# Performance work log

Measured on AMD Instinct MI355X. Metric: run time of the kernel, lower is better.

Reference implementation:

```python
import jax, jax.numpy as jnp
import numpy as np

# Config (matches init_kwargs)
D_MODEL = 1024
D_MLP = 4096
N_EXPERTS = 8
TOP_K = 2  # experts_per_token
BATCH = 1
POS = 2048


def setup_inputs() -> dict:
    key = jax.random.key(0)
    k0, k1, k2, k3, k4 = jax.random.split(key, 5)
    s = 0.02  # typical init scale
    x = jax.random.normal(k0, (BATCH, POS, D_MODEL), jnp.float32)
    W_gate = jax.random.normal(k1, (D_MODEL, N_EXPERTS), jnp.float32) * s  # router
    We_gate = jax.random.normal(k2, (N_EXPERTS, D_MODEL, D_MLP), jnp.float32) * s
    We_in = jax.random.normal(k3, (N_EXPERTS, D_MODEL, D_MLP), jnp.float32) * s
    We_out = jax.random.normal(k4, (N_EXPERTS, D_MLP, D_MODEL), jnp.float32) * s
    return {"x": x, "W_gate": W_gate, "We_gate": We_gate, "We_in": We_in, "We_out": We_out}


def reference(x, W_gate, We_gate, We_in, We_out):
    B, P, D = x.shape
    T = B * P
    E = W_gate.shape[1]
    h = x.reshape(T, D)  # [T, D]

    # Router: logits -> fp32 softmax -> top-k -> renormalize (as in torch code)
    logits = h @ W_gate  # [T, E]
    probs = jax.nn.softmax(logits.astype(jnp.float32), axis=-1)
    topw, topi = jax.lax.top_k(probs, TOP_K)  # [T, K]
    topw = topw / jnp.sum(topw, axis=-1, keepdims=True)
    topw = topw.astype(x.dtype)

    # Per-token combine weight for each expert (0 if not routed). [T, E]
    w_full = jnp.zeros((T, E), x.dtype).at[jnp.arange(T)[:, None], topi].add(topw)

    # Gated-MLP per expert; scan over the small fixed expert axis to avoid
    # materializing [E, T, D_MLP] hidden states at once.
    def per_expert(acc, params):
        Wg, Wi, Wo, we = params  # Wg/Wi: [D, D_MLP], Wo: [D_MLP, D], we: [T]
        hid = jax.nn.silu(h @ Wg) * (h @ Wi)  # [T, D_MLP]
        return acc + (hid @ Wo) * we[:, None], None

    res, _ = jax.lax.scan(
        per_expert,
        jnp.zeros((T, D), x.dtype),
        (We_gate, We_in, We_out, w_full.T),
    )
    return res.reshape(B, P, D)
```

## Files before the change

### kernel.cpp

```cpp
#include <hip/hip_runtime.h>
#include <hip/hip_bf16.h>

#define T_TOK 2048
#define DMODEL 1024
#define DMLP 4096
#define NEXP 8

typedef __bf16 bf16x8 __attribute__((ext_vector_type(8)));
typedef float f32x4 __attribute__((ext_vector_type(4)));

__device__ __forceinline__ unsigned short f2bf(float f) {
  return __builtin_bit_cast(unsigned short, (__bf16)f);
}

__device__ __forceinline__ void gload16(const unsigned short* g,
                                        unsigned short* l) {
  __builtin_amdgcn_global_load_lds(
      (const __attribute__((address_space(1))) unsigned int*)g,
      (__attribute__((address_space(3))) unsigned int*)l, 16, 0, 0);
}

__global__ __launch_bounds__(64) void router_k(
    const float* __restrict__ x, const float* __restrict__ wg,
    int* __restrict__ topi, float* __restrict__ topw,
    unsigned short* __restrict__ xb) {
  int t = blockIdx.x;
  int lane = threadIdx.x;
  const float* hx = x + (size_t)t * DMODEL;
  float acc[NEXP];
#pragma unroll
  for (int e = 0; e < NEXP; ++e) acc[e] = 0.f;
  for (int i = lane; i < DMODEL; i += 64) {
    float xi = hx[i];
    if (xb) xb[(size_t)t * DMODEL + i] = f2bf(xi);
    const float* w = wg + (size_t)i * NEXP;
#pragma unroll
    for (int e = 0; e < NEXP; ++e) acc[e] += xi * w[e];
  }
#pragma unroll
  for (int off = 32; off > 0; off >>= 1) {
#pragma unroll
    for (int e = 0; e < NEXP; ++e) acc[e] += __shfl_down(acc[e], off);
  }
  if (lane == 0) {
    float m = acc[0];
#pragma unroll
    for (int e = 1; e < NEXP; ++e) m = fmaxf(m, acc[e]);
    float p[NEXP], s = 0.f;
#pragma unroll
    for (int e = 0; e < NEXP; ++e) { p[e] = expf(acc[e] - m); s += p[e]; }
    float inv = 1.f / s;
#pragma unroll
    for (int e = 0; e < NEXP; ++e) p[e] *= inv;
    int i1 = 0;
#pragma unroll
    for (int e = 1; e < NEXP; ++e) if (p[e] > p[i1]) i1 = e;
    int i2 = (i1 == 0) ? 1 : 0;
#pragma unroll
    for (int e = 0; e < NEXP; ++e) if (e != i1 && p[e] > p[i2]) i2 = e;
    float w1 = p[i1], w2 = p[i2];
    float rs = 1.f / (w1 + w2);
    topi[2 * t] = i1;
    topi[2 * t + 1] = i2;
    topw[2 * t] = w1 * rs;
    topw[2 * t + 1] = w2 * rs;
  }
}

__global__ __launch_bounds__(512) void compact_k(
    const int* __restrict__ topi, const float* __restrict__ topw,
    int* __restrict__ offsets, int* __restrict__ perm,
    float* __restrict__ wrow, int* __restrict__ inv) {
  int tid = threadIdx.x;
  int e = tid >> 6, lane = tid & 63;
  __shared__ unsigned char st[2 * T_TOK];
  __shared__ int scnt[NEXP];
  __shared__ int soff[NEXP + 1];
  for (int i = tid; i < (2 * T_TOK) / 4; i += 512) {
    int4 v = ((const int4*)topi)[i];
    uchar4 u;
    u.x = (unsigned char)v.x; u.y = (unsigned char)v.y;
    u.z = (unsigned char)v.z; u.w = (unsigned char)v.w;
    ((uchar4*)st)[i] = u;
  }
  __syncthreads();
  int c = 0;
  for (int j = lane; j < 2 * T_TOK; j += 64) {
    unsigned long long m = __ballot(st[j] == e);
    c += __popcll(m);
  }
  if (lane == 0) scnt[e] = c;
  __syncthreads();
  if (tid == 0) {
    int s = 0;
    for (int k = 0; k < NEXP; ++k) { soff[k] = s; s += scnt[k]; }
    soff[NEXP] = s;
    for (int k = 0; k <= NEXP; ++k) offsets[k] = soff[k];
  }
  __syncthreads();
  int base = soff[e];
  for (int j = lane; j < 2 * T_TOK; j += 64) {
    bool f = (st[j] == e);
    unsigned long long m = __ballot(f);
    if (f) {
      int p = base + __popcll(m & ((1ULL << lane) - 1ULL));
      perm[p] = j >> 1;
      wrow[p] = topw[j];
      inv[j] = p;
    }
    base += __popcll(m);
  }
}

template <int SK, int SN>
__global__ __launch_bounds__(256) void tpose_k(
    const float* __restrict__ src0, unsigned short* __restrict__ dst0) {
  int e = blockIdx.z;
  const float* src = src0 + (size_t)e * SK * SN;
  unsigned short* dst = dst0 + (size_t)e * SK * SN;
  int k0 = blockIdx.y * 64, c0 = blockIdx.x * 64;
  __shared__ unsigned short tl[64 * 64];
  int tid = threadIdx.x;
  int j = tid & 15, g = tid >> 4;
  int c4 = j * 4, r0 = g * 4;
  const float* sp = src + (size_t)(k0 + r0) * SN + c0 + c4;
  float4 v0 = *(const float4*)(sp);
  float4 v1 = *(const float4*)(sp + SN);
  float4 v2 = *(const float4*)(sp + 2 * SN);
  float4 v3 = *(const float4*)(sp + 3 * SN);
  const float* p0 = (const float*)&v0;
  const float* p1 = (const float*)&v1;
  const float* p2 = (const float*)&v2;
  const float* p3 = (const float*)&v3;
#pragma unroll
  for (int i = 0; i < 4; ++i) {
    int c = c4 + i;
    ushort4 u;
    u.x = f2bf(p0[i]); u.y = f2bf(p1[i]);
    u.z = f2bf(p2[i]); u.w = f2bf(p3[i]);
    int sw = ((c >> 2) & 14) << 2;
    *(ushort4*)(&tl[c * 64 + (r0 ^ sw)]) = u;
  }
  __syncthreads();
#pragma unroll
  for (int i = 0; i < 2; ++i) {
    int task = tid + i * 256;
    int rr = task >> 3, cc = task & 7;
    int sw = ((rr >> 2) & 14) << 2;
    uint4 w = *(const uint4*)(&tl[rr * 64 + ((cc * 8) ^ sw)]);
    *(uint4*)(dst + (size_t)(c0 + rr) * SK + k0 + cc * 8) = w;
  }
}

__global__ __launch_bounds__(256) void hid2_k(
    const unsigned short* __restrict__ xb, const unsigned short* __restrict__ wgt,
    const unsigned short* __restrict__ wit, const int* __restrict__ offsets,
    const int* __restrict__ perm, const float* __restrict__ wrow,
    unsigned short* __restrict__ hid) {
  int e = blockIdx.z;
  int off = offsets[e], end = offsets[e + 1];
  int cnt = end - off;
  int m0 = blockIdx.y * 128;
  if (m0 >= cnt) return;
  int nb = blockIdx.x * 64;

  __shared__ unsigned short As[128 * 32];
  __shared__ unsigned short Bs[128 * 32];

  int tid = threadIdx.x;
  int lane = tid & 63, wid = tid >> 6;
  int wm = (wid & 1) * 64, wn = (wid >> 1) * 64;
  int lr = lane & 15, q = lane >> 4;

  f32x4 acc[4][4];
  f32x4 z = {0.f, 0.f, 0.f, 0.f};
#pragma unroll
  for (int i = 0; i < 4; ++i)
#pragma unroll
    for (int j = 0; j < 4; ++j) acc[i][j] = z;

  const unsigned short* aptr[2];
  const unsigned short* bptr[2];
#pragma unroll
  for (int it = 0; it < 2; ++it) {
    int task = tid + it * 256;
    int r = task >> 2, ch = task & 3;
    int pl = m0 + r;
    int src = perm[off + ((pl < cnt) ? pl : 0)];
    aptr[it] = xb + (size_t)src * DMODEL + ch * 8;
    int arr = (r >> 5) & 1;
    int col = nb + (r & 31) + ((r >> 6) << 5);
    const unsigned short* w =
        (arr ? wit : wgt) + (size_t)e * DMLP * DMODEL;
    bptr[it] = w + (size_t)col * DMODEL + ch * 8;
  }

  for (int k0 = 0; k0 < DMODEL; k0 += 32) {
#pragma unroll
    for (int it = 0; it < 2; ++it) {
      gload16(aptr[it] + k0, &As[(tid + it * 256) * 8]);
      gload16(bptr[it] + k0, &Bs[(tid + it * 256) * 8]);
    }
    __syncthreads();
    bf16x8 af[4], bfr[4];
#pragma unroll
    for (int i = 0; i < 4; ++i)
      af[i] = *(const bf16x8*)(&As[(wm + i * 16 + lr) * 32 + q * 8]);
#pragma unroll
    for (int j = 0; j < 4; ++j)
      bfr[j] = *(const bf16x8*)(&Bs[(wn + j * 16 + lr) * 32 + q * 8]);
#pragma unroll
    for (int i = 0; i < 4; ++i)
#pragma unroll
      for (int j = 0; j < 4; ++j)
        acc[i][j] = __builtin_amdgcn_mfma_f32_16x16x32_bf16(af[i], bfr[j],
                                                            acc[i][j], 0, 0, 0);
    __syncthreads();
  }

  int colbase = nb + (wn ? 32 : 0);
#pragma unroll
  for (int i = 0; i < 4; ++i) {
#pragma unroll
    for (int jp = 0; jp < 2; ++jp) {
#pragma unroll
      for (int r = 0; r < 4; ++r) {
        int row = wm + i * 16 + q * 4 + r;
        int pl = m0 + row;
        if (pl < cnt) {
          int pos = off + pl;
          float g = acc[i][jp][r], vv = acc[i][jp + 2][r];
          float hv = (g / (1.f + expf(-g))) * vv * wrow[pos];
          hid[(size_t)pos * DMLP + colbase + jp * 16 + lr] = f2bf(hv);
        }
      }
    }
  }
}

__global__ __launch_bounds__(256) void out2_k(
    const unsigned short* __restrict__ hid, const unsigned short* __restrict__ wot,
    const int* __restrict__ offsets, float* __restrict__ tmp) {
  int e = blockIdx.z;
  int off = offsets[e], end = offsets[e + 1];
  int cnt = end - off;
  int m0 = blockIdx.y * 128;
  if (m0 >= cnt) return;
  int n0 = blockIdx.x * 128;

  __shared__ unsigned short As[128 * 32];
  __shared__ unsigned short Bs[128 * 32];

  int tid = threadIdx.x;
  int lane = tid & 63, wid = tid >> 6;
  int wm = (wid & 1) * 64, wn = (wid >> 1) * 64;
  int lr = lane & 15, q = lane >> 4;

  f32x4 acc[4][4];
  f32x4 z = {0.f, 0.f, 0.f, 0.f};
#pragma unroll
  for (int i = 0; i < 4; ++i)
#pragma unroll
    for (int j = 0; j < 4; ++j) acc[i][j] = z;

  const unsigned short* aptr[2];
  const unsigned short* bptr[2];
#pragma unroll
  for (int it = 0; it < 2; ++it) {
    int task = tid + it * 256;
    int r = task >> 2, ch = task & 3;
    int pl = m0 + r;
    aptr[it] = hid + (size_t)(off + ((pl < cnt) ? pl : 0)) * DMLP + ch * 8;
    bptr[it] = wot + (size_t)e * DMODEL * DMLP + (size_t)(n0 + r) * DMLP + ch * 8;
  }

  for (int k0 = 0; k0 < DMLP; k0 += 32) {
#pragma unroll
    for (int it = 0; it < 2; ++it) {
      gload16(aptr[it] + k0, &As[(tid + it * 256) * 8]);
      gload16(bptr[it] + k0, &Bs[(tid + it * 256) * 8]);
    }
    __syncthreads();
    bf16x8 af[4], bfr[4];
#pragma unroll
    for (int i = 0; i < 4; ++i)
      af[i] = *(const bf16x8*)(&As[(wm + i * 16 + lr) * 32 + q * 8]);
#pragma unroll
    for (int j = 0; j < 4; ++j)
      bfr[j] = *(const bf16x8*)(&Bs[(wn + j * 16 + lr) * 32 + q * 8]);
#pragma unroll
    for (int i = 0; i < 4; ++i)
#pragma unroll
      for (int j = 0; j < 4; ++j)
        acc[i][j] = __builtin_amdgcn_mfma_f32_16x16x32_bf16(af[i], bfr[j],
                                                            acc[i][j], 0, 0, 0);
    __syncthreads();
  }

#pragma unroll
  for (int i = 0; i < 4; ++i)
#pragma unroll
    for (int j = 0; j < 4; ++j)
#pragma unroll
      for (int r = 0; r < 4; ++r) {
        int row = wm + i * 16 + q * 4 + r;
        int pl = m0 + row;
        if (pl < cnt) {
          tmp[(size_t)(off + pl) * DMODEL + n0 + wn + j * 16 + lr] =
              acc[i][j][r];
        }
      }
}

__global__ __launch_bounds__(256) void comb_k(const float* __restrict__ tmp,
                                              const int* __restrict__ inv,
                                              float* __restrict__ out) {
  int t = blockIdx.x, c = threadIdx.x;
  int i0 = inv[2 * t], i1 = inv[2 * t + 1];
  const float4* t4 = (const float4*)tmp;
  float4 a = t4[(size_t)i0 * 256 + c];
  float4 b = t4[(size_t)i1 * 256 + c];
  float4 o;
  o.x = a.x + b.x; o.y = a.y + b.y; o.z = a.z + b.z; o.w = a.w + b.w;
  ((float4*)out)[(size_t)t * 256 + c] = o;
}

#define BPITCH 40

__global__ __launch_bounds__(256) void hid_k(
    const float* __restrict__ x, const float* __restrict__ weg,
    const float* __restrict__ wei, const int* __restrict__ offsets,
    const int* __restrict__ perm, const float* __restrict__ wrow,
    unsigned short* __restrict__ hid) {
  int e = blockIdx.z;
  int off = offsets[e], end = offsets[e + 1];
  int cnt = end - off;
  int m0 = blockIdx.y * 128;
  if (m0 >= cnt) return;
  int nb = blockIdx.x * 64;
  const float* wg = weg + (size_t)e * DMODEL * DMLP;
  const float* wi = wei + (size_t)e * DMODEL * DMLP;

  __shared__ unsigned short As[128 * BPITCH];
  __shared__ unsigned short Bg[64 * BPITCH];
  __shared__ unsigned short Bi[64 * BPITCH];

  int tid = threadIdx.x;
  int lane = tid & 63, wid = tid >> 6;
  int wm = (wid & 1) * 64, wn = (wid >> 1) * 32;
  int lr = lane & 15, q = lane >> 4;

  f32x4 accg[4][2], acci[4][2];
  f32x4 z = {0.f, 0.f, 0.f, 0.f};
#pragma unroll
  for (int i = 0; i < 4; ++i)
#pragma unroll
    for (int j = 0; j < 2; ++j) { accg[i][j] = z; acci[i][j] = z; }

  const float* aptr[4];
  int adst[4];
#pragma unroll
  for (int it = 0; it < 4; ++it) {
    int task = tid + it * 256;
    int r = task >> 3, kc = (task & 7) * 4;
    int pl = m0 + r;
    int src = perm[off + ((pl < cnt) ? pl : 0)];
    aptr[it] = x + (size_t)src * DMODEL + kc;
    adst[it] = r * BPITCH + kc;
  }
  int tn = (tid & 15) * 4, tk = (tid >> 4) * 2;

  for (int k0 = 0; k0 < DMODEL; k0 += 32) {
#pragma unroll
    for (int it = 0; it < 4; ++it) {
      float4 v = *(const float4*)(aptr[it] + k0);
      ushort4 u;
      u.x = f2bf(v.x); u.y = f2bf(v.y); u.z = f2bf(v.z); u.w = f2bf(v.w);
      *(ushort4*)(&As[adst[it]]) = u;
    }
    {
      const float* pg = wg + (size_t)(k0 + tk) * DMLP + nb + tn;
      float4 g0 = *(const float4*)(pg);
      float4 g1 = *(const float4*)(pg + DMLP);
      const float* pi = wi + (size_t)(k0 + tk) * DMLP + nb + tn;
      float4 i0 = *(const float4*)(pi);
      float4 i1 = *(const float4*)(pi + DMLP);
      const float* c0 = (const float*)&g0;
      const float* c1 = (const float*)&g1;
      const float* d0 = (const float*)&i0;
      const float* d1 = (const float*)&i1;
#pragma unroll
      for (int cix = 0; cix < 4; ++cix) {
        ushort2 vg; vg.x = f2bf(c0[cix]); vg.y = f2bf(c1[cix]);
        *(ushort2*)(&Bg[(tn + cix) * BPITCH + tk]) = vg;
        ushort2 vi; vi.x = f2bf(d0[cix]); vi.y = f2bf(d1[cix]);
        *(ushort2*)(&Bi[(tn + cix) * BPITCH + tk]) = vi;
      }
    }
    __syncthreads();
    bf16x8 af[4], bgf[2], bif[2];
#pragma unroll
    for (int i = 0; i < 4; ++i)
      af[i] = *(const bf16x8*)(&As[(wm + i * 16 + lr) * BPITCH + q * 8]);
#pragma unroll
    for (int j = 0; j < 2; ++j) {
      bgf[j] = *(const bf16x8*)(&Bg[(wn + j * 16 + lr) * BPITCH + q * 8]);
      bif[j] = *(const bf16x8*)(&Bi[(wn + j * 16 + lr) * BPITCH + q * 8]);
    }
#pragma unroll
    for (int i = 0; i < 4; ++i)
#pragma unroll
      for (int j = 0; j < 2; ++j) {
        accg[i][j] = __builtin_amdgcn_mfma_f32_16x16x32_bf16(af[i], bgf[j], accg[i][j], 0, 0, 0);
        acci[i][j] = __builtin_amdgcn_mfma_f32_16x16x32_bf16(af[i], bif[j], acci[i][j], 0, 0, 0);
      }
    __syncthreads();
  }
#pragma unroll
  for (int i = 0; i < 4; ++i)
#pragma unroll
    for (int j = 0; j < 2; ++j)
#pragma unroll
      for (int r = 0; r < 4; ++r) {
        int row = wm + i * 16 + q * 4 + r;
        int pl = m0 + row;
        if (pl < cnt) {
          int pos = off + pl;
          float g = accg[i][j][r], vv = acci[i][j][r];
          float hv = (g / (1.f + expf(-g))) * vv * wrow[pos];
          hid[(size_t)pos * DMLP + nb + wn + j * 16 + lr] = f2bf(hv);
        }
      }
}

__global__ __launch_bounds__(256) void out_k(
    const unsigned short* __restrict__ hid, const float* __restrict__ weo,
    const int* __restrict__ offsets, const int* __restrict__ perm,
    float* __restrict__ out) {
  int e = blockIdx.z;
  int off = offsets[e], end = offsets[e + 1];
  int cnt = end - off;
  int m0 = blockIdx.y * 128;
  if (m0 >= cnt) return;
  int nb = blockIdx.x * 64;
  const float* wo = weo + (size_t)e * DMLP * DMODEL;

  __shared__ unsigned short As[128 * BPITCH];
  __shared__ unsigned short Bs[64 * BPITCH];

  int tid = threadIdx.x;
  int lane = tid & 63, wid = tid >> 6;
  int wm = (wid & 1) * 64, wn = (wid >> 1) * 32;
  int lr = lane & 15, q = lane >> 4;

  f32x4 acc[4][2];
  f32x4 z = {0.f, 0.f, 0.f, 0.f};
#pragma unroll
  for (int i = 0; i < 4; ++i)
#pragma unroll
    for (int j = 0; j < 2; ++j) acc[i][j] = z;

  const unsigned short* aptr[2];
  int adst[2];
#pragma unroll
  for (int it = 0; it < 2; ++it) {
    int task = tid + it * 256;
    int r = task >> 2, kg = (task & 3) * 8;
    int pl = m0 + r;
    int src = off + ((pl < cnt) ? pl : 0);
    aptr[it] = hid + (size_t)src * DMLP + kg;
    adst[it] = r * BPITCH + kg;
  }
  int tn = (tid & 15) * 4, tk = (tid >> 4) * 2;

  for (int k0 = 0; k0 < DMLP; k0 += 32) {
#pragma unroll
    for (int it = 0; it < 2; ++it) {
      uint4 v = *(const uint4*)(aptr[it] + k0);
      *(uint4*)(&As[adst[it]]) = v;
    }
    {
      const float* pb = wo + (size_t)(k0 + tk) * DMODEL + nb + tn;
      float4 b0 = *(const float4*)(pb);
      float4 b1 = *(const float4*)(pb + DMODEL);
      const float* c0 = (const float*)&b0;
      const float* c1 = (const float*)&b1;
#pragma unroll
      for (int cix = 0; cix < 4; ++cix) {
        ushort2 vb; vb.x = f2bf(c0[cix]); vb.y = f2bf(c1[cix]);
        *(ushort2*)(&Bs[(tn + cix) * BPITCH + tk]) = vb;
      }
    }
    __syncthreads();
    bf16x8 af[4], bf[2];
#pragma unroll
    for (int i = 0; i < 4; ++i)
      af[i] = *(const bf16x8*)(&As[(wm + i * 16 + lr) * BPITCH + q * 8]);
#pragma unroll
    for (int j = 0; j < 2; ++j)
      bf[j] = *(const bf16x8*)(&Bs[(wn + j * 16 + lr) * BPITCH + q * 8]);
#pragma unroll
    for (int i = 0; i < 4; ++i)
#pragma unroll
      for (int j = 0; j < 2; ++j)
        acc[i][j] = __builtin_amdgcn_mfma_f32_16x16x32_bf16(af[i], bf[j], acc[i][j], 0, 0, 0);
    __syncthreads();
  }
#pragma unroll
  for (int i = 0; i < 4; ++i)
#pragma unroll
    for (int j = 0; j < 2; ++j)
#pragma unroll
      for (int r = 0; r < 4; ++r) {
        int row = wm + i * 16 + q * 4 + r;
        int pl = m0 + row;
        if (pl < cnt) {
          int tok = perm[off + pl];
          atomicAdd(&out[(size_t)tok * DMODEL + nb + wn + j * 16 + lr],
                    acc[i][j][r]);
        }
      }
}

extern "C" void kernel_launch(void* const* d_in, const int* in_sizes, int n_in,
                              void* d_out, int out_size, void* d_ws,
                              size_t ws_size, hipStream_t stream) {
  const float* x = (const float*)d_in[0];
  const float* wgate = (const float*)d_in[1];
  const float* weg = (const float*)d_in[2];
  const float* wei = (const float*)d_in[3];
  const float* weo = (const float*)d_in[4];
  float* out = (float*)d_out;

  char* ws = (char*)d_ws;
  const size_t KB = 1024, MB = 1048576;
  int* topi = (int*)(ws + 0 * KB);
  float* topw = (float*)(ws + 16 * KB);
  int* offsets = (int*)(ws + 32 * KB);
  int* perm = (int*)(ws + 33 * KB);
  float* wrow = (float*)(ws + 49 * KB);
  int* inv = (int*)(ws + 65 * KB);

  bool big = ws_size >= (size_t)245 * MB;
  unsigned short* xb = big ? (unsigned short*)(ws + 1 * MB) : nullptr;

  router_k<<<dim3(T_TOK), dim3(64), 0, stream>>>(x, wgate, topi, topw, xb);
  compact_k<<<dim3(1), dim3(512), 0, stream>>>(topi, topw, offsets, perm, wrow, inv);

  if (big) {
    unsigned short* hid = (unsigned short*)(ws + 5 * MB);
    float* tmp = (float*)(ws + 37 * MB);
    unsigned short* wgt = (unsigned short*)(ws + 53 * MB);
    unsigned short* wit = (unsigned short*)(ws + 117 * MB);
    unsigned short* wot = (unsigned short*)(ws + 181 * MB);

    tpose_k<DMODEL, DMLP><<<dim3(DMLP / 64, DMODEL / 64, NEXP), dim3(256), 0,
                            stream>>>(weg, wgt);
    tpose_k<DMODEL, DMLP><<<dim3(DMLP / 64, DMODEL / 64, NEXP), dim3(256), 0,
                            stream>>>(wei, wit);
    tpose_k<DMLP, DMODEL><<<dim3(DMODEL / 64, DMLP / 64, NEXP), dim3(256), 0,
                            stream>>>(weo, wot);
    hid2_k<<<dim3(DMLP / 64, T_TOK / 128, NEXP), dim3(256), 0, stream>>>(
        xb, wgt, wit, offsets, perm, wrow, hid);
    out2_k<<<dim3(DMODEL / 128, T_TOK / 128, NEXP), dim3(256), 0, stream>>>(
        hid, wot, offsets, tmp);
    comb_k<<<dim3(T_TOK), dim3(256), 0, stream>>>(tmp, inv, out);
  } else {
    unsigned short* hid = (unsigned short*)(ws + 96 * KB);
    hipMemsetAsync(d_out, 0, (size_t)out_size * sizeof(float), stream);
    hid_k<<<dim3(DMLP / 64, T_TOK / 128, NEXP), dim3(256), 0, stream>>>(
        x, weg, wei, offsets, perm, wrow, hid);
    out_k<<<dim3(DMODEL / 64, T_TOK / 128, NEXP), dim3(256), 0, stream>>>(
        hid, weo, offsets, perm, out);
  }
}
```

Before: 664.4 us.

## Fuse weight transposes, swizzle GEMM LDS layout, halve out-GEMM N tile

```diff
diff --git a/kernel.cpp b/kernel.cpp
--- a/kernel.cpp
+++ b/kernel.cpp
@@ -8,6 +8,7 @@
 
 typedef __bf16 bf16x8 __attribute__((ext_vector_type(8)));
 typedef float f32x4 __attribute__((ext_vector_type(4)));
+typedef unsigned short u16x8 __attribute__((ext_vector_type(8)));
 
 __device__ __forceinline__ unsigned short f2bf(float f) {
   return __builtin_bit_cast(unsigned short, (__bf16)f);
@@ -112,42 +113,50 @@
   }
 }
 
-template <int SK, int SN>
-__global__ __launch_bounds__(256) void tpose_k(
-    const float* __restrict__ src0, unsigned short* __restrict__ dst0) {
-  int e = blockIdx.z;
-  const float* src = src0 + (size_t)e * SK * SN;
-  unsigned short* dst = dst0 + (size_t)e * SK * SN;
-  int k0 = blockIdx.y * 64, c0 = blockIdx.x * 64;
+__global__ __launch_bounds__(256) void tpose3_k(
+    const float* __restrict__ weg, const float* __restrict__ wei,
+    const float* __restrict__ weo, unsigned short* __restrict__ wgt,
+    unsigned short* __restrict__ wit, unsigned short* __restrict__ wot) {
+  int mat = blockIdx.z;
+  int e = blockIdx.y;
+  const float* src;
+  unsigned short* dst;
+  int SK, SN;
+  if (mat == 0) { src = weg; dst = wgt; SK = DMODEL; SN = DMLP; }
+  else if (mat == 1) { src = wei; dst = wit; SK = DMODEL; SN = DMLP; }
+  else { src = weo; dst = wot; SK = DMLP; SN = DMODEL; }
+  src += (size_t)e * DMODEL * DMLP;
+  dst += (size_t)e * DMODEL * DMLP;
+  int ntx = SN >> 6;
+  int tile = blockIdx.x;
+  int c0 = (tile & (ntx - 1)) * 64, k0 = (tile / ntx) * 64;
+
   __shared__ unsigned short tl[64 * 64];
   int tid = threadIdx.x;
-  int j = tid & 15, g = tid >> 4;
-  int c4 = j * 4, r0 = g * 4;
-  const float* sp = src + (size_t)(k0 + r0) * SN + c0 + c4;
-  float4 v0 = *(const float4*)(sp);
-  float4 v1 = *(const float4*)(sp + SN);
-  float4 v2 = *(const float4*)(sp + 2 * SN);
-  float4 v3 = *(const float4*)(sp + 3 * SN);
-  const float* p0 = (const float*)&v0;
-  const float* p1 = (const float*)&v1;
-  const float* p2 = (const float*)&v2;
-  const float* p3 = (const float*)&v3;
-#pragma unroll
-  for (int i = 0; i < 4; ++i) {
-    int c = c4 + i;
-    ushort4 u;
-    u.x = f2bf(p0[i]); u.y = f2bf(p1[i]);
-    u.z = f2bf(p2[i]); u.w = f2bf(p3[i]);
-    int sw = ((c >> 2) & 14) << 2;
-    *(ushort4*)(&tl[c * 64 + (r0 ^ sw)]) = u;
+  int j = tid & 31, g = tid >> 5;
+  int r0 = g * 8;
+
+  const float* sp = src + (size_t)(k0 + r0) * SN + c0 + 2 * j;
+  float2 v[8];
+#pragma unroll
+  for (int ri = 0; ri < 8; ++ri) v[ri] = *(const float2*)(sp + (size_t)ri * SN);
+#pragma unroll
+  for (int i = 0; i < 2; ++i) {
+    int cc = 2 * j + i;
+    u16x8 p;
+#pragma unroll
+    for (int ri = 0; ri < 8; ++ri)
+      p[ri] = f2bf(i ? v[ri].y : v[ri].x);
+    int sl = (g + cc) & 7;
+    *(u16x8*)(&tl[cc * 64 + sl * 8]) = p;
   }
   __syncthreads();
 #pragma unroll
   for (int i = 0; i < 2; ++i) {
     int task = tid + i * 256;
     int rr = task >> 3, cc = task & 7;
-    int sw = ((rr >> 2) & 14) << 2;
-    uint4 w = *(const uint4*)(&tl[rr * 64 + ((cc * 8) ^ sw)]);
+    int sl = (cc + rr) & 7;
+    uint4 w = *(const uint4*)(&tl[rr * 64 + sl * 8]);
     *(uint4*)(dst + (size_t)(c0 + rr) * SK + k0 + cc * 8) = w;
   }
 }
@@ -184,14 +193,14 @@
 #pragma unroll
   for (int it = 0; it < 2; ++it) {
     int task = tid + it * 256;
-    int r = task >> 2, ch = task & 3;
+    int r = task >> 2, sp4 = task & 3;
+    int ch = (sp4 - (r >> 1)) & 3;
     int pl = m0 + r;
     int src = perm[off + ((pl < cnt) ? pl : 0)];
     aptr[it] = xb + (size_t)src * DMODEL + ch * 8;
     int arr = (r >> 5) & 1;
     int col = nb + (r & 31) + ((r >> 6) << 5);
-    const unsigned short* w =
-        (arr ? wit : wgt) + (size_t)e * DMLP * DMODEL;
+    const unsigned short* w = (arr ? wit : wgt) + (size_t)e * DMLP * DMODEL;
     bptr[it] = w + (size_t)col * DMODEL + ch * 8;
   }
 
@@ -204,11 +213,15 @@
     __syncthreads();
     bf16x8 af[4], bfr[4];
 #pragma unroll
-    for (int i = 0; i < 4; ++i)
-      af[i] = *(const bf16x8*)(&As[(wm + i * 16 + lr) * 32 + q * 8]);
-#pragma unroll
-    for (int j = 0; j < 4; ++j)
-      bfr[j] = *(const bf16x8*)(&Bs[(wn + j * 16 + lr) * 32 + q * 8]);
+    for (int i = 0; i < 4; ++i) {
+      int R = wm + i * 16 + lr;
+      af[i] = *(const bf16x8*)(&As[R * 32 + (((q + (R >> 1)) & 3) * 8)]);
+    }
+#pragma unroll
+    for (int j = 0; j < 4; ++j) {
+      int R = wn + j * 16 + lr;
+      bfr[j] = *(const bf16x8*)(&Bs[R * 32 + (((q + (R >> 1)) & 3) * 8)]);
+    }
 #pragma unroll
     for (int i = 0; i < 4; ++i)
 #pragma unroll
@@ -246,52 +259,60 @@
   int cnt = end - off;
   int m0 = blockIdx.y * 128;
   if (m0 >= cnt) return;
-  int n0 = blockIdx.x * 128;
+  int n0 = blockIdx.x * 64;
 
   __shared__ unsigned short As[128 * 32];
-  __shared__ unsigned short Bs[128 * 32];
+  __shared__ unsigned short Bs[64 * 32];
 
   int tid = threadIdx.x;
   int lane = tid & 63, wid = tid >> 6;
-  int wm = (wid & 1) * 64, wn = (wid >> 1) * 64;
+  int wm = (wid & 1) * 64, wn = (wid >> 1) * 32;
   int lr = lane & 15, q = lane >> 4;
 
-  f32x4 acc[4][4];
+  f32x4 acc[4][2];
   f32x4 z = {0.f, 0.f, 0.f, 0.f};
 #pragma unroll
   for (int i = 0; i < 4; ++i)
 #pragma unroll
-    for (int j = 0; j < 4; ++j) acc[i][j] = z;
+    for (int j = 0; j < 2; ++j) acc[i][j] = z;
 
   const unsigned short* aptr[2];
-  const unsigned short* bptr[2];
+  const unsigned short* bptr;
 #pragma unroll
   for (int it = 0; it < 2; ++it) {
     int task = tid + it * 256;
-    int r = task >> 2, ch = task & 3;
+    int r = task >> 2, sp4 = task & 3;
+    int ch = (sp4 - (r >> 1)) & 3;
     int pl = m0 + r;
     aptr[it] = hid + (size_t)(off + ((pl < cnt) ? pl : 0)) * DMLP + ch * 8;
-    bptr[it] = wot + (size_t)e * DMODEL * DMLP + (size_t)(n0 + r) * DMLP + ch * 8;
+  }
+  {
+    int r = tid >> 2, sp4 = tid & 3;
+    int ch = (sp4 - (r >> 1)) & 3;
+    bptr = wot + (size_t)e * DMODEL * DMLP + (size_t)(n0 + r) * DMLP + ch * 8;
   }
 
   for (int k0 = 0; k0 < DMLP; k0 += 32) {
 #pragma unroll
-    for (int it = 0; it < 2; ++it) {
+    for (int it = 0; it < 2; ++it)
       gload16(aptr[it] + k0, &As[(tid + it * 256) * 8]);
-      gload16(bptr[it] + k0, &Bs[(tid + it * 256) * 8]);
-    }
-    __syncthreads();
-    bf16x8 af[4], bfr[4];
+    gload16(bptr + k0, &Bs[tid * 8]);
+    __syncthreads();
+    bf16x8 af[4], bfr[2];
+#pragma unroll
+    for (int i = 0; i < 4; ++i) {
+      int R = wm + i * 16 + lr;
+      af[i] = *(const bf16x8*)(&As[R * 32 + (((q + (R >> 1)) & 3) * 8)]);
+    }
+#pragma unroll
+    for (int j = 0; j < 2; ++j) {
+      int R = wn + j * 16 + lr;
+      bfr[j] = *(const bf16x8*)(&Bs[R * 32 + (((q + (R >> 1)) & 3) * 8)]);
+    }
 #pragma unroll
     for (int i = 0; i < 4; ++i)
-      af[i] = *(const bf16x8*)(&As[(wm + i * 16 + lr) * 32 + q * 8]);
-#pragma unroll
-    for (int j = 0; j < 4; ++j)
-      bfr[j] = *(const bf16x8*)(&Bs[(wn + j * 16 + lr) * 32 + q * 8]);
-#pragma unroll
-    for (int i = 0; i < 4; ++i)
-#pragma unroll
-      for (int j = 0; j < 4; ++j)
+#pragma unroll
+      for (int j = 0; j < 2; ++j)
         acc[i][j] = __builtin_amdgcn_mfma_f32_16x16x32_bf16(af[i], bfr[j],
                                                             acc[i][j], 0, 0, 0);
     __syncthreads();
@@ -300,7 +321,7 @@
 #pragma unroll
   for (int i = 0; i < 4; ++i)
 #pragma unroll
-    for (int j = 0; j < 4; ++j)
+    for (int j = 0; j < 2; ++j)
 #pragma unroll
       for (int r = 0; r < 4; ++r) {
         int row = wm + i * 16 + q * 4 + r;
@@ -554,15 +575,11 @@
     unsigned short* wit = (unsigned short*)(ws + 117 * MB);
     unsigned short* wot = (unsigned short*)(ws + 181 * MB);
 
-    tpose_k<DMODEL, DMLP><<<dim3(DMLP / 64, DMODEL / 64, NEXP), dim3(256), 0,
-                            stream>>>(weg, wgt);
-    tpose_k<DMODEL, DMLP><<<dim3(DMLP / 64, DMODEL / 64, NEXP), dim3(256), 0,
-                            stream>>>(wei, wit);
-    tpose_k<DMLP, DMODEL><<<dim3(DMODEL / 64, DMLP / 64, NEXP), dim3(256), 0,
-                            stream>>>(weo, wot);
+    tpose3_k<<<dim3(1024, NEXP, 3), dim3(256), 0, stream>>>(weg, wei, weo,
+                                                            wgt, wit, wot);
     hid2_k<<<dim3(DMLP / 64, T_TOK / 128, NEXP), dim3(256), 0, stream>>>(
         xb, wgt, wit, offsets, perm, wrow, hid);
-    out2_k<<<dim3(DMODEL / 128, T_TOK / 128, NEXP), dim3(256), 0, stream>>>(
+    out2_k<<<dim3(DMODEL / 64, T_TOK / 128, NEXP), dim3(256), 0, stream>>>(
         hid, wot, offsets, tmp);
     comb_k<<<dim3(T_TOK), dim3(256), 0, stream>>>(tmp, inv, out);
   } else {
```

New measurement: 661.4 us. About the same (-0.4%).
